# Performance work log

Hardware: AMD Instinct MI355X
Metric: run time of the kernel (lower is better)

The kernel has to match this reference:

```python
import jax, jax.numpy as jnp
import numpy as np

EMBED_DIM = 1024
NUM_HEADS = 16
HEAD_DIM = EMBED_DIM // NUM_HEADS
SCALE = HEAD_DIM ** -0.5
B, L = 1, 4096


def setup_inputs() -> dict:
    key = jax.random.key(0)
    ks = jax.random.split(key, 10)
    init = 1.0 / np.sqrt(EMBED_DIM)  # rough Linear-like init scale
    inp = {
        "hidden_states": jax.random.normal(ks[0], (B, L, EMBED_DIM), dtype=jnp.float32),
        # ToMe token sizes: >= 1 so log(size) is finite
        "size": jax.random.uniform(ks[1], (B, 1, L), dtype=jnp.float32) + 1.0,
        "wq": jax.random.normal(ks[2], (EMBED_DIM, EMBED_DIM), dtype=jnp.float32) * init,
        "bq": jax.random.normal(ks[3], (EMBED_DIM,), dtype=jnp.float32) * init,
        "wk": jax.random.normal(ks[4], (EMBED_DIM, EMBED_DIM), dtype=jnp.float32) * init,
        "bk": jax.random.normal(ks[5], (EMBED_DIM,), dtype=jnp.float32) * init,
        "wv": jax.random.normal(ks[6], (EMBED_DIM, EMBED_DIM), dtype=jnp.float32) * init,
        "bv": jax.random.normal(ks[7], (EMBED_DIM,), dtype=jnp.float32) * init,
        "wo": jax.random.normal(ks[8], (EMBED_DIM, EMBED_DIM), dtype=jnp.float32) * init,
        "bo": jax.random.normal(ks[9], (EMBED_DIM,), dtype=jnp.float32) * init,
    }
    return inp


def reference(hidden_states, size, wq, bq, wk, bk, wv, bv, wo, bo):
    b, t, d = hidden_states.shape
    h, hd = NUM_HEADS, HEAD_DIM

    def heads(x):  # (b, t, d) -> (b, h, t, hd)
        return x.reshape(b, t, h, hd).transpose(0, 2, 1, 3)

    q = heads((hidden_states @ wq.T + bq) * SCALE)
    k = heads(hidden_states @ wk.T + bk)
    v = heads(hidden_states @ wv.T + bv)

    metric = k.mean(axis=1)  # (b, t, hd): per-token key averaged over heads

    logits = jnp.einsum('bhqd,bhkd->bhqk', q, k)
    # size: (b, 1, src) -> log-size bias broadcast over heads and queries
    logits = logits + jnp.log(size)[:, None, :, :]
    probs = jax.nn.softmax(logits, axis=-1)  # dropout p=0 (eval)

    attn = jnp.einsum('bhqk,bhkd->bhqd', probs, v)
    attn = attn.transpose(0, 2, 1, 3).reshape(b, t, d)
    out = attn @ wo.T + bo
    return out, metric
```

## Files before the change

### kernel.cpp

```cpp
#include <hip/hip_runtime.h>

static constexpr int L_SEQ = 4096;
static constexpr int EMBED = 1024;
static constexpr int HEADS = 16;
static constexpr int HD    = 64;

typedef unsigned short ushortT;
typedef __attribute__((ext_vector_type(8)))  short short8;
typedef __attribute__((ext_vector_type(4)))  float f32x4;
typedef __attribute__((ext_vector_type(4)))  unsigned uint4v;

#define LOG2E 1.4426950408889634f

__device__ __forceinline__ ushortT f2bf(float f) {
  unsigned u = __builtin_bit_cast(unsigned, f);
  u += 0x7fffu + ((u >> 16) & 1u);
  return (ushortT)(u >> 16);
}
__device__ __forceinline__ float bf2f(ushortT s) {
  return __builtin_bit_cast(float, ((unsigned)s) << 16);
}
__device__ __forceinline__ unsigned cvtpk(float a, float b) {
  unsigned r;
  asm("v_cvt_pk_bf16_f32 %0, %1, %2" : "=v"(r) : "v"(a), "v"(b));
  return r;
}

#define GLOAD_LDS16(g, l) \
  __builtin_amdgcn_global_load_lds((const __attribute__((address_space(1))) void*)(g), \
                                   (__attribute__((address_space(3))) void*)(l), 16, 0, 0)

__global__ void cast_bf16_k(const float* __restrict__ in, ushortT* __restrict__ out, int n8) {
  int i = blockIdx.x * blockDim.x + threadIdx.x;
  if (i >= n8) return;
  const float4* p = (const float4*)in;
  float4 a = p[2 * i], b = p[2 * i + 1];
  uint4 o;
  o.x = (unsigned)f2bf(a.x) | ((unsigned)f2bf(a.y) << 16);
  o.y = (unsigned)f2bf(a.z) | ((unsigned)f2bf(a.w) << 16);
  o.z = (unsigned)f2bf(b.x) | ((unsigned)f2bf(b.y) << 16);
  o.w = (unsigned)f2bf(b.z) | ((unsigned)f2bf(b.w) << 16);
  ((uint4*)out)[i] = o;
}

__global__ void cast4_bf16_k(const float* __restrict__ a, const float* __restrict__ b,
                             const float* __restrict__ c, const float* __restrict__ d,
                             ushortT* __restrict__ out) {
  int idx = blockIdx.x * blockDim.x + threadIdx.x;
  int w = idx >> 17, i = idx & 131071;
  const float* src = (w == 0) ? a : (w == 1) ? b : (w == 2) ? c : d;
  const float4* p = (const float4*)src;
  float4 x = p[2 * i], y = p[2 * i + 1];
  uint4 o;
  o.x = (unsigned)f2bf(x.x) | ((unsigned)f2bf(x.y) << 16);
  o.y = (unsigned)f2bf(x.z) | ((unsigned)f2bf(x.w) << 16);
  o.z = (unsigned)f2bf(y.x) | ((unsigned)f2bf(y.y) << 16);
  o.w = (unsigned)f2bf(y.z) | ((unsigned)f2bf(y.w) << 16);
  ((uint4*)(out + ((size_t)w << 20)))[i] = o;
}

__global__ void l2size_k(const float* __restrict__ sz, float* __restrict__ l2s, int n) {
  int i = blockIdx.x * blockDim.x + threadIdx.x;
  if (i < n) l2s[i] = __log2f(sz[i]);
}

struct GemmArgs { const ushortT* B; const float* bias; void* dst; int mode; };

__global__ __launch_bounds__(256, 3) void gemm_bt_k(
    const ushortT* __restrict__ A, GemmArgs g0, GemmArgs g1, GemmArgs g2)
{
  constexpr int K = 1024;
  __shared__ __align__(16) ushortT As[128 * 64];
  __shared__ __align__(16) ushortT Bs[128 * 64];

  GemmArgs g = (blockIdx.y == 0) ? g0 : ((blockIdx.y == 1) ? g1 : g2);
  const ushortT* __restrict__ Bw = g.B;

  const int tid = threadIdx.x;
  const int wv = tid >> 6, ln = tid & 63;
  const int nb = blockIdx.x & 7, mb = blockIdx.x >> 3;
  const int m0 = mb * 128, n0 = nb * 128;
  const int wr = wv >> 1, wc = wv & 1;
  const int lrow = ln & 15, lq = ln >> 4;

  const int rstg = wv * 8 + (ln >> 3);
  const int ustg = (ln & 7) ^ (ln >> 3);

  f32x4 acc[4][4] = {};

  for (int kt = 0; kt < K; kt += 64) {
#pragma unroll
    for (int i = 0; i < 4; ++i) {
      int r = i * 32 + rstg;
      GLOAD_LDS16(A  + (size_t)(m0 + r) * K + kt + (ustg << 3), As + i * 2048 + wv * 512);
      GLOAD_LDS16(Bw + (size_t)(n0 + r) * K + kt + (ustg << 3), Bs + i * 2048 + wv * 512);
    }
    __syncthreads();
#pragma unroll
    for (int ks = 0; ks < 2; ++ks) {
      short8 a[4], b[4];
#pragma unroll
      for (int mi = 0; mi < 4; ++mi) {
        int ra = wr * 64 + mi * 16 + lrow;
        int u = (ks * 4 + lq) ^ (ra & 7);
        a[mi] = *(const short8*)(As + ra * 64 + (u << 3));
      }
#pragma unroll
      for (int ni = 0; ni < 4; ++ni) {
        int rb = wc * 64 + ni * 16 + lrow;
        int u = (ks * 4 + lq) ^ (rb & 7);
        b[ni] = *(const short8*)(Bs + rb * 64 + (u << 3));
      }
#pragma unroll
      for (int mi = 0; mi < 4; ++mi)
#pragma unroll
        for (int ni = 0; ni < 4; ++ni)
          acc[mi][ni] = __builtin_amdgcn_mfma_f32_16x16x32_bf16(a[mi], b[ni], acc[mi][ni], 0, 0, 0);
    }
    __syncthreads();
  }

  const int mode = g.mode;
  if (mode <= 1) {
    ushortT* dst = (ushortT*)g.dst;
    const float sc = (mode == 0) ? 0.125f : 1.0f;
#pragma unroll
    for (int ni = 0; ni < 4; ++ni) {
      int n = n0 + wc * 64 + ni * 16 + lrow;
      float bsv = g.bias[n];
      size_t base = ((size_t)(n >> 6) * L_SEQ) * HD + (n & 63);
#pragma unroll
      for (int mi = 0; mi < 4; ++mi)
#pragma unroll
        for (int r = 0; r < 4; ++r) {
          int m = m0 + wr * 64 + mi * 16 + lq * 4 + r;
          dst[base + (size_t)m * HD] = f2bf((acc[mi][ni][r] + bsv) * sc);
        }
    }
  } else if (mode == 2) {
    ushortT* dst = (ushortT*)g.dst;
#pragma unroll
    for (int ni = 0; ni < 4; ++ni) {
      int n = n0 + wc * 64 + ni * 16 + lrow;
      float bsv = g.bias[n];
      size_t base = (size_t)n * L_SEQ;
#pragma unroll
      for (int mi = 0; mi < 4; ++mi)
#pragma unroll
        for (int r = 0; r < 4; ++r) {
          int m = m0 + wr * 64 + mi * 16 + lq * 4 + r;
          dst[base + m] = f2bf(acc[mi][ni][r] + bsv);
        }
    }
  } else {
    float* dst = (float*)g.dst;
#pragma unroll
    for (int ni = 0; ni < 4; ++ni) {
      int n = n0 + wc * 64 + ni * 16 + lrow;
      float bsv = g.bias[n];
#pragma unroll
      for (int mi = 0; mi < 4; ++mi)
#pragma unroll
        for (int r = 0; r < 4; ++r) {
          int m = m0 + wr * 64 + mi * 16 + lq * 4 + r;
          dst[(size_t)m * EMBED + n] = acc[mi][ni][r] + bsv;
        }
    }
  }
}

__global__ __launch_bounds__(512, 4) void attn_k(
    const ushortT* __restrict__ Q,
    const ushortT* __restrict__ Kb,
    const ushortT* __restrict__ Vt,
    const float*   __restrict__ l2s,
    ushortT* __restrict__ O)
{
  __shared__ __align__(16) ushortT Ks[2][2][64 * 64];
  __shared__ __align__(16) ushortT Vs[2][2][64 * 64];

  const int id = blockIdx.x;
  const int xcd = id & 7, s = id >> 3;
  const int h  = xcd * 2 + (s >> 5);
  const int q0 = (s & 31) * 128;

  const int tid = threadIdx.x;
  const int wv  = tid >> 6;
  const int grp = wv >> 2, wvg = wv & 3;
  const int ln  = tid & 63;
  const int lrow = ln & 15, lq = ln >> 4;

  short8 qf[2][2];
#pragma unroll
  for (int hf = 0; hf < 2; ++hf) {
    const ushortT* qp = Q + ((size_t)h * L_SEQ + q0 + wvg * 32 + hf * 16 + lrow) * HD + lq * 8;
    qf[hf][0] = *(const short8*)qp;
    qf[hf][1] = *(const short8*)(qp + 32);
  }

  f32x4 o0[4] = {}, o1[4] = {};
  float mrun0 = -1e30f, lrun0 = 0.f;
  float mrun1 = -1e30f, lrun1 = 0.f;

  const int rstg = wvg * 8 + (ln >> 3);
  const int ustg = (ln & 7) ^ (ln >> 3);

  const ushortT* kbase = Kb + ((size_t)h * L_SEQ + rstg) * HD + (ustg << 3);
  const ushortT* vbase = Vt + ((size_t)(h * HD) + rstg) * L_SEQ + (ustg << 3);

  auto STAGE = [&](int buf, int kt) {
    const int t0 = kt * 64;
#pragma unroll
    for (int i = 0; i < 2; ++i) {
      GLOAD_LDS16(kbase + t0 * 64 + i * (32 * HD), &Ks[grp][buf][i * 2048 + wvg * 512]);
      GLOAD_LDS16(vbase + t0 + i * (32 * L_SEQ),   &Vs[grp][buf][i * 2048 + wvg * 512]);
    }
  };

  const int sw = lrow & 7;
  const int vo0 = lrow * 128 + ((((lq >> 1))     ^ sw) << 4) + (lq & 1) * 8;
  const int vo1 = lrow * 128 + ((((lq >> 1) + 2) ^ sw) << 4) + (lq & 1) * 8;
  const int vo2 = lrow * 128 + ((((lq >> 1) + 4) ^ sw) << 4) + (lq & 1) * 8;
  const int vo3 = lrow * 128 + ((((lq >> 1) + 6) ^ sw) << 4) + (lq & 1) * 8;

  const int tbase = grp * 32;
  STAGE(0, tbase);
  __syncthreads();

#pragma unroll 1
  for (int t = 0; t < 32; ++t) {
    const int cur = t & 1;
    if (t + 1 < 32) STAGE(cur ^ 1, tbase + t + 1);
    const int t0 = (tbase + t) * 64;
    const ushortT* Kt = &Ks[grp][cur][0];
    const char*    Vb = (const char*)&Vs[grp][cur][0];

    f32x4 s0[4] = {}, s1[4] = {};
    __builtin_amdgcn_s_setprio(1);
#pragma unroll
    for (int ks = 0; ks < 2; ++ks) {
#pragma unroll
      for (int f = 0; f < 4; ++f) {
        int key = f * 16 + lrow;
        int u = (ks * 4 + lq) ^ (key & 7);
        short8 kb = *(const short8*)(Kt + key * 64 + (u << 3));
        s0[f] = __builtin_amdgcn_mfma_f32_16x16x32_bf16(kb, qf[0][ks], s0[f], 0, 0, 0);
        s1[f] = __builtin_amdgcn_mfma_f32_16x16x32_bf16(kb, qf[1][ks], s1[f], 0, 0, 0);
      }
    }
    __builtin_amdgcn_s_setprio(0);

#pragma unroll
    for (int f = 0; f < 4; ++f) {
      f32x4 b = *(const f32x4*)(l2s + t0 + f * 16 + lq * 4);
#pragma unroll
      for (int r = 0; r < 4; ++r) {
        s0[f][r] = s0[f][r] * LOG2E + b[r];
        s1[f][r] = s1[f][r] * LOG2E + b[r];
      }
    }

    float pm0 = fmaxf(fmaxf(fmaxf(s0[0][0], s0[0][1]), fmaxf(s0[0][2], s0[0][3])),
                      fmaxf(fmaxf(s0[1][0], s0[1][1]), fmaxf(s0[1][2], s0[1][3])));
    pm0 = fmaxf(pm0, fmaxf(fmaxf(fmaxf(s0[2][0], s0[2][1]), fmaxf(s0[2][2], s0[2][3])),
                           fmaxf(fmaxf(s0[3][0], s0[3][1]), fmaxf(s0[3][2], s0[3][3]))));
    float pm1 = fmaxf(fmaxf(fmaxf(s1[0][0], s1[0][1]), fmaxf(s1[0][2], s1[0][3])),
                      fmaxf(fmaxf(s1[1][0], s1[1][1]), fmaxf(s1[1][2], s1[1][3])));
    pm1 = fmaxf(pm1, fmaxf(fmaxf(fmaxf(s1[2][0], s1[2][1]), fmaxf(s1[2][2], s1[2][3])),
                           fmaxf(fmaxf(s1[3][0], s1[3][1]), fmaxf(s1[3][2], s1[3][3]))));
    pm0 = fmaxf(pm0, __shfl_xor(pm0, 16));
    pm0 = fmaxf(pm0, __shfl_xor(pm0, 32));
    pm1 = fmaxf(pm1, __shfl_xor(pm1, 16));
    pm1 = fmaxf(pm1, __shfl_xor(pm1, 32));
    float mnew0  = fmaxf(mrun0, pm0);
    float mnew1  = fmaxf(mrun1, pm1);
    float alpha0 = __builtin_amdgcn_exp2f(mrun0 - mnew0);
    float alpha1 = __builtin_amdgcn_exp2f(mrun1 - mnew1);
    mrun0 = mnew0; mrun1 = mnew1;

    float rs0 = 0.f, rs1 = 0.f;
#pragma unroll
    for (int f = 0; f < 4; ++f)
#pragma unroll
      for (int r = 0; r < 4; ++r) {
        float pv0 = __builtin_amdgcn_exp2f(s0[f][r] - mrun0);
        float pv1 = __builtin_amdgcn_exp2f(s1[f][r] - mrun1);
        s0[f][r] = pv0; rs0 += pv0;
        s1[f][r] = pv1; rs1 += pv1;
      }
    rs0 += __shfl_xor(rs0, 16);
    rs0 += __shfl_xor(rs0, 32);
    rs1 += __shfl_xor(rs1, 16);
    rs1 += __shfl_xor(rs1, 32);
    lrun0 = lrun0 * alpha0 + rs0;
    lrun1 = lrun1 * alpha1 + rs1;

    if (!__all(alpha0 == 1.0f && alpha1 == 1.0f)) {
#pragma unroll
      for (int df = 0; df < 4; ++df)
#pragma unroll
        for (int r = 0; r < 4; ++r) {
          o0[df][r] *= alpha0;
          o1[df][r] *= alpha1;
        }
    }

    short8 pb00, pb10, pb01, pb11;
    {
      unsigned a0 = cvtpk(s0[0][0], s0[0][1]), a1 = cvtpk(s0[0][2], s0[0][3]);
      unsigned a2 = cvtpk(s0[1][0], s0[1][1]), a3 = cvtpk(s0[1][2], s0[1][3]);
      unsigned a4 = cvtpk(s0[2][0], s0[2][1]), a5 = cvtpk(s0[2][2], s0[2][3]);
      unsigned a6 = cvtpk(s0[3][0], s0[3][1]), a7 = cvtpk(s0[3][2], s0[3][3]);
      pb00 = __builtin_bit_cast(short8, (uint4v){a0, a1, a2, a3});
      pb10 = __builtin_bit_cast(short8, (uint4v){a4, a5, a6, a7});
      unsigned b0 = cvtpk(s1[0][0], s1[0][1]), b1 = cvtpk(s1[0][2], s1[0][3]);
      unsigned b2 = cvtpk(s1[1][0], s1[1][1]), b3 = cvtpk(s1[1][2], s1[1][3]);
      unsigned b4 = cvtpk(s1[2][0], s1[2][1]), b5 = cvtpk(s1[2][2], s1[2][3]);
      unsigned b6 = cvtpk(s1[3][0], s1[3][1]), b7 = cvtpk(s1[3][2], s1[3][3]);
      pb01 = __builtin_bit_cast(short8, (uint4v){b0, b1, b2, b3});
      pb11 = __builtin_bit_cast(short8, (uint4v){b4, b5, b6, b7});
    }

    __builtin_amdgcn_s_setprio(1);
#pragma unroll
    for (int df = 0; df < 4; ++df) {
      const char* vr = Vb + df * 2048;
      uint2 a0 = *(const uint2*)(vr + vo0);
      uint2 a1 = *(const uint2*)(vr + vo1);
      short8 va = __builtin_bit_cast(short8, (uint4v){a0.x, a0.y, a1.x, a1.y});
      o0[df] = __builtin_amdgcn_mfma_f32_16x16x32_bf16(va, pb00, o0[df], 0, 0, 0);
      o1[df] = __builtin_amdgcn_mfma_f32_16x16x32_bf16(va, pb01, o1[df], 0, 0, 0);
      uint2 a2 = *(const uint2*)(vr + vo2);
      uint2 a3 = *(const uint2*)(vr + vo3);
      short8 vb2 = __builtin_bit_cast(short8, (uint4v){a2.x, a2.y, a3.x, a3.y});
      o0[df] = __builtin_amdgcn_mfma_f32_16x16x32_bf16(vb2, pb10, o0[df], 0, 0, 0);
      o1[df] = __builtin_amdgcn_mfma_f32_16x16x32_bf16(vb2, pb11, o1[df], 0, 0, 0);
    }
    __builtin_amdgcn_s_setprio(0);

    __syncthreads();
  }

  float* Ob = (float*)&Ks[0][0][0];
  float* Ml = (float*)&Vs[0][0][0];
  const int ql0 = wvg * 32 + lrow;

  if (grp == 1) {
#pragma unroll
    for (int df = 0; df < 4; ++df) {
      *(f32x4*)(Ob + ql0 * 64 + df * 16 + lq * 4)        = o0[df];
      *(f32x4*)(Ob + (ql0 + 16) * 64 + df * 16 + lq * 4) = o1[df];
    }
    Ml[ql0 * 2] = mrun0;        Ml[ql0 * 2 + 1] = lrun0;
    Ml[(ql0 + 16) * 2] = mrun1; Ml[(ql0 + 16) * 2 + 1] = lrun1;
  }
  __syncthreads();
  if (grp == 0) {
    {
      float m1 = Ml[ql0 * 2], l1 = Ml[ql0 * 2 + 1];
      float m  = fmaxf(mrun0, m1);
      float w0 = __builtin_amdgcn_exp2f(mrun0 - m);
      float w1 = __builtin_amdgcn_exp2f(m1 - m);
      float inv = 1.0f / (lrun0 * w0 + l1 * w1);
      ushortT* ob = O + (size_t)(q0 + ql0) * EMBED + h * HD;
#pragma unroll
      for (int df = 0; df < 4; ++df) {
        f32x4 p1 = *(const f32x4*)(Ob + ql0 * 64 + df * 16 + lq * 4);
        uint2 w;
        w.x = (unsigned)f2bf((o0[df][0] * w0 + p1[0] * w1) * inv) |
              ((unsigned)f2bf((o0[df][1] * w0 + p1[1] * w1) * inv) << 16);
        w.y = (unsigned)f2bf((o0[df][2] * w0 + p1[2] * w1) * inv) |
              ((unsigned)f2bf((o0[df][3] * w0 + p1[3] * w1) * inv) << 16);
        *(uint2*)(ob + df * 16 + lq * 4) = w;
      }
    }
    {
      float m1 = Ml[(ql0 + 16) * 2], l1 = Ml[(ql0 + 16) * 2 + 1];
      float m  = fmaxf(mrun1, m1);
      float w0 = __builtin_amdgcn_exp2f(mrun1 - m);
      float w1 = __builtin_amdgcn_exp2f(m1 - m);
      float inv = 1.0f / (lrun1 * w0 + l1 * w1);
      ushortT* ob = O + (size_t)(q0 + ql0 + 16) * EMBED + h * HD;
#pragma unroll
      for (int df = 0; df < 4; ++df) {
        f32x4 p1 = *(const f32x4*)(Ob + (ql0 + 16) * 64 + df * 16 + lq * 4);
        uint2 w;
        w.x = (unsigned)f2bf((o1[df][0] * w0 + p1[0] * w1) * inv) |
              ((unsigned)f2bf((o1[df][1] * w0 + p1[1] * w1) * inv) << 16);
        w.y = (unsigned)f2bf((o1[df][2] * w0 + p1[2] * w1) * inv) |
              ((unsigned)f2bf((o1[df][3] * w0 + p1[3] * w1) * inv) << 16);
        *(uint2*)(ob + df * 16 + lq * 4) = w;
      }
    }
  }
}

__global__ void metric_k(const ushortT* __restrict__ Kb, float* __restrict__ out) {
  int idx = blockIdx.x * blockDim.x + threadIdx.x;
  int t = idx >> 3, c8 = idx & 7;
  float acc[8] = {};
#pragma unroll
  for (int h = 0; h < HEADS; ++h) {
    short8 v = *(const short8*)(Kb + ((size_t)h * L_SEQ + t) * HD + c8 * 8);
#pragma unroll
    for (int j = 0; j < 8; ++j) acc[j] += bf2f((ushortT)v[j]);
  }
  float* dst = out + (size_t)t * HD + c8 * 8;
#pragma unroll
  for (int j = 0; j < 8; ++j) dst[j] = acc[j] * (1.0f / 16.0f);
}

extern "C" void kernel_launch(void* const* d_in, const int* in_sizes, int n_in,
                              void* d_out, int out_size, void* d_ws, size_t ws_size,
                              hipStream_t stream) {
  const float* hs = (const float*)d_in[0];
  const float* sz = (const float*)d_in[1];
  const float* wq = (const float*)d_in[2];
  const float* bq = (const float*)d_in[3];
  const float* wk = (const float*)d_in[4];
  const float* bk = (const float*)d_in[5];
  const float* wv = (const float*)d_in[6];
  const float* bv = (const float*)d_in[7];
  const float* wo = (const float*)d_in[8];
  const float* bo = (const float*)d_in[9];

  char* ws = (char*)d_ws;
  ushortT* hs_b = (ushortT*)(ws);
  ushortT* wq_b = (ushortT*)(ws + (8u << 20));
  ushortT* wk_b = wq_b + (1u << 20);
  ushortT* wv_b = wq_b + (2u << 20);
  ushortT* wo_b = wq_b + (3u << 20);
  ushortT* q_b  = (ushortT*)(ws + (16u << 20));
  ushortT* k_b  = (ushortT*)(ws + (24u << 20));
  ushortT* vt_b = (ushortT*)(ws + (32u << 20));
  ushortT* at_b = (ushortT*)(ws + (40u << 20));
  float*   l2s  = (float*)(ws + (48u << 20));

  float* outp    = (float*)d_out;
  float* metricp = outp + (size_t)L_SEQ * EMBED;

  cast_bf16_k<<<L_SEQ * EMBED / 8 / 256, 256, 0, stream>>>(hs, hs_b, L_SEQ * EMBED / 8);
  cast4_bf16_k<<<2048, 256, 0, stream>>>(wq, wk, wv, wo, wq_b);
  l2size_k<<<L_SEQ / 256, 256, 0, stream>>>(sz, l2s, L_SEQ);

  GemmArgs aq{wq_b, bq, (void*)q_b, 0};
  GemmArgs ak{wk_b, bk, (void*)k_b, 1};
  GemmArgs av{wv_b, bv, (void*)vt_b, 2};
  gemm_bt_k<<<dim3(256, 3), 256, 0, stream>>>(hs_b, aq, ak, av);

  metric_k<<<L_SEQ * 8 / 256, 256, 0, stream>>>(k_b, metricp);

  attn_k<<<512, 512, 0, stream>>>(q_b, k_b, vt_b, l2s, at_b);

  GemmArgs ao{wo_b, bo, (void*)outp, 3};
  gemm_bt_k<<<dim3(256, 1), 256, 0, stream>>>(at_b, ao, ao, ao);
}
```

Before: 185.3 us.

## Fold log2e into Q scale, preload bias into MFMA accumulators, add 64-row out-proj GEMM

The Q projection now scales by 0.125*log2e, so the attention kernel can start its score accumulators from the log2-size bias. That removes the per-element multiply-add after QK^T. The output projection moves to a dedicated GEMM with 64x128 tiles and 512 blocks instead of 256 blocks of 128x128, to fill more CUs on the final GEMM. The trade-off is lower per-block reuse and a small numerical shift from rounding the scaled Q to bf16.

```diff
diff --git a/kernel.cpp b/kernel.cpp
--- a/kernel.cpp
+++ b/kernel.cpp
@@ -123,7 +123,7 @@
   const int mode = g.mode;
   if (mode <= 1) {
     ushortT* dst = (ushortT*)g.dst;
-    const float sc = (mode == 0) ? 0.125f : 1.0f;
+    const float sc = (mode == 0) ? (0.125f * LOG2E) : 1.0f;
 #pragma unroll
     for (int ni = 0; ni < 4; ++ni) {
       int n = n0 + wc * 64 + ni * 16 + lrow;
@@ -137,7 +137,7 @@
           dst[base + (size_t)m * HD] = f2bf((acc[mi][ni][r] + bsv) * sc);
         }
     }
-  } else if (mode == 2) {
+  } else {
     ushortT* dst = (ushortT*)g.dst;
 #pragma unroll
     for (int ni = 0; ni < 4; ++ni) {
@@ -152,20 +152,76 @@
           dst[base + m] = f2bf(acc[mi][ni][r] + bsv);
         }
     }
-  } else {
-    float* dst = (float*)g.dst;
-#pragma unroll
-    for (int ni = 0; ni < 4; ++ni) {
-      int n = n0 + wc * 64 + ni * 16 + lrow;
-      float bsv = g.bias[n];
-#pragma unroll
-      for (int mi = 0; mi < 4; ++mi)
-#pragma unroll
-        for (int r = 0; r < 4; ++r) {
-          int m = m0 + wr * 64 + mi * 16 + lq * 4 + r;
-          dst[(size_t)m * EMBED + n] = acc[mi][ni][r] + bsv;
-        }
-    }
+  }
+}
+
+__global__ __launch_bounds__(256, 2) void gemm_o64_k(
+    const ushortT* __restrict__ A, const ushortT* __restrict__ Bw,
+    const float* __restrict__ bias, float* __restrict__ dst)
+{
+  constexpr int K = 1024;
+  __shared__ __align__(16) ushortT As[64 * 64];
+  __shared__ __align__(16) ushortT Bs[128 * 64];
+
+  const int tid = threadIdx.x;
+  const int wv = tid >> 6, ln = tid & 63;
+  const int nb = blockIdx.x & 7, mb = blockIdx.x >> 3;
+  const int m0 = mb * 64, n0 = nb * 128;
+  const int wr = wv >> 1, wc = wv & 1;
+  const int lrow = ln & 15, lq = ln >> 4;
+
+  const int rstg = wv * 8 + (ln >> 3);
+  const int ustg = (ln & 7) ^ (ln >> 3);
+
+  f32x4 acc[2][4] = {};
+
+  for (int kt = 0; kt < K; kt += 64) {
+#pragma unroll
+    for (int i = 0; i < 2; ++i) {
+      int r = i * 32 + rstg;
+      GLOAD_LDS16(A + (size_t)(m0 + r) * K + kt + (ustg << 3), As + i * 2048 + wv * 512);
+    }
+#pragma unroll
+    for (int i = 0; i < 4; ++i) {
+      int r = i * 32 + rstg;
+      GLOAD_LDS16(Bw + (size_t)(n0 + r) * K + kt + (ustg << 3), Bs + i * 2048 + wv * 512);
+    }
+    __syncthreads();
+#pragma unroll
+    for (int ks = 0; ks < 2; ++ks) {
+      short8 a[2], b[4];
+#pragma unroll
+      for (int mi = 0; mi < 2; ++mi) {
+        int ra = wr * 32 + mi * 16 + lrow;
+        int u = (ks * 4 + lq) ^ (ra & 7);
+        a[mi] = *(const short8*)(As + ra * 64 + (u << 3));
+      }
+#pragma unroll
+      for (int ni = 0; ni < 4; ++ni) {
+        int rb = wc * 64 + ni * 16 + lrow;
+        int u = (ks * 4 + lq) ^ (rb & 7);
+        b[ni] = *(const short8*)(Bs + rb * 64 + (u << 3));
+      }
+#pragma unroll
+      for (int mi = 0; mi < 2; ++mi)
+#pragma unroll
+        for (int ni = 0; ni < 4; ++ni)
+          acc[mi][ni] = __builtin_amdgcn_mfma_f32_16x16x32_bf16(a[mi], b[ni], acc[mi][ni], 0, 0, 0);
+    }
+    __syncthreads();
+  }
+
+#pragma unroll
+  for (int ni = 0; ni < 4; ++ni) {
+    int n = n0 + wc * 64 + ni * 16 + lrow;
+    float bsv = bias[n];
+#pragma unroll
+    for (int mi = 0; mi < 2; ++mi)
+#pragma unroll
+      for (int r = 0; r < 4; ++r) {
+        int m = m0 + wr * 32 + mi * 16 + lq * 4 + r;
+        dst[(size_t)m * EMBED + n] = acc[mi][ni][r] + bsv;
+      }
   }
 }
 
@@ -235,7 +291,13 @@
     const ushortT* Kt = &Ks[grp][cur][0];
     const char*    Vb = (const char*)&Vs[grp][cur][0];
 
-    f32x4 s0[4] = {}, s1[4] = {};
+    f32x4 s0[4], s1[4];
+#pragma unroll
+    for (int f = 0; f < 4; ++f) {
+      f32x4 b = *(const f32x4*)(l2s + t0 + f * 16 + lq * 4);
+      s0[f] = b; s1[f] = b;
+    }
+
     __builtin_amdgcn_s_setprio(1);
 #pragma unroll
     for (int ks = 0; ks < 2; ++ks) {
@@ -249,16 +311,6 @@
       }
     }
     __builtin_amdgcn_s_setprio(0);
-
-#pragma unroll
-    for (int f = 0; f < 4; ++f) {
-      f32x4 b = *(const f32x4*)(l2s + t0 + f * 16 + lq * 4);
-#pragma unroll
-      for (int r = 0; r < 4; ++r) {
-        s0[f][r] = s0[f][r] * LOG2E + b[r];
-        s1[f][r] = s1[f][r] * LOG2E + b[r];
-      }
-    }
 
     float pm0 = fmaxf(fmaxf(fmaxf(s0[0][0], s0[0][1]), fmaxf(s0[0][2], s0[0][3])),
                       fmaxf(fmaxf(s0[1][0], s0[1][1]), fmaxf(s0[1][2], s0[1][3])));
@@ -452,6 +504,5 @@
 
   attn_k<<<512, 512, 0, stream>>>(q_b, k_b, vt_b, l2s, at_b);
 
-  GemmArgs ao{wo_b, bo, (void*)outp, 3};
-  gemm_bt_k<<<dim3(256, 1), 256, 0, stream>>>(at_b, ao, ao, ao);
-}
+  gemm_o64_k<<<512, 256, 0, stream>>>(at_b, wo_b, bo, outp);
+}
```

After: 179.1 us. 3.3% less time.
